# Kernel optimization log

Hardware: AMD Instinct MI355X
Metric: run time of the kernel (lower is better)

The kernel has to match this reference:

```python
import jax, jax.numpy as jnp
import numpy as np

N = 100000   # num_nodes
E = 1600000  # num_edges
H = 128      # hidden_dim
OUT = 1      # output_dim
SLOPE = 0.2  # GATConv leaky_relu negative_slope


def setup_inputs() -> dict:
    key = jax.random.key(0)
    ks = jax.random.split(key, 10)
    s = 1.0 / np.sqrt(H)
    return {
        "h": jnp.arange(N, dtype=jnp.int64 if jax.config.jax_enable_x64 else jnp.int32),
        "edge_index": jax.random.randint(ks[0], (2, E), 0, N),
        "node_type": jax.random.randint(ks[1], (N,), 0, 3),
        "emb": jax.random.normal(ks[2], (N, H), jnp.float32) * s,
        "W1": jax.random.normal(ks[3], (H, H), jnp.float32) * s,
        "a_src1": jax.random.normal(ks[4], (H,), jnp.float32) * s,
        "a_dst1": jax.random.normal(ks[5], (H,), jnp.float32) * s,
        "b1": jnp.zeros((H,), jnp.float32),
        "W2": jax.random.normal(ks[6], (H, OUT), jnp.float32) * s,
        "a_src2": jax.random.normal(ks[7], (OUT,), jnp.float32) * s,
        "a_dst2": jax.random.normal(ks[8], (OUT,), jnp.float32) * s,
        "b2": jnp.zeros((OUT,), jnp.float32),
    }


def gat_layer(x, src, dst, emask, W, a_src, a_dst, b, n_nodes):
    """PyG GATConv (heads=1, add_self_loops=True). Masked edges get -inf logits."""
    xp = x @ W                                  # [N, F]
    e_src = xp @ a_src                          # [N]
    e_dst = xp @ a_dst                          # [N]
    logits = jax.nn.leaky_relu(e_src[src] + e_dst[dst], SLOPE)   # [E]
    logits = jnp.where(emask, logits, -jnp.inf)
    self_logits = jax.nn.leaky_relu(e_src + e_dst, SLOPE)        # [N] self-loops
    # segment softmax over destination nodes (edges + self loop)
    m = jax.ops.segment_max(logits, dst, num_segments=n_nodes)
    m = jnp.maximum(m, self_logits)             # finite: self loop always present
    ew = jnp.exp(logits - m[dst])               # masked edges -> exp(-inf)=0
    sw = jnp.exp(self_logits - m)
    denom = jax.ops.segment_sum(ew, dst, num_segments=n_nodes) + sw
    alpha = ew / denom[dst]                     # [E]
    alpha_self = sw / denom                     # [N]
    out = jax.ops.segment_sum(alpha[:, None] * xp[src], dst, num_segments=n_nodes)
    out = out + alpha_self[:, None] * xp + b
    return out


def reference(h, edge_index, node_type, emb, W1, a_src1, a_dst1, b1, W2, a_src2, a_dst2, b2):
    src, dst = edge_index[0], edge_index[1]
    emask = (node_type[src] == 0) & (node_type[dst] == 0)
    x = emb[h]                                          # embedding lookup [N, H]
    x = gat_layer(x, src, dst, emask, W1, a_src1, a_dst1, b1, emb.shape[0])
    x = jax.nn.relu(x)
    x = gat_layer(x, src, dst, emask, W2, a_src2, a_dst2, b2, emb.shape[0])
    return x
```

## Files before the change

kernel.cpp:

```cpp
#include <hip/hip_runtime.h>

#define N_NODES 100000
#define N_EDGES 1600000
#define HD 128
#define SLOPE 0.2f
#define NBLK 391
#define GB 782
#define EB3 1563
#define CAP 32
#define SLICE_LD 136

typedef __attribute__((ext_vector_type(8))) short bf16x8;
typedef __attribute__((ext_vector_type(4))) float f32x4;

__device__ __forceinline__ unsigned short f2bf(float f) {
    union { float f; unsigned u; } v; v.f = f;
    const unsigned u = v.u + 0x7FFFu + ((v.u >> 16) & 1u);
    return (unsigned short)(u >> 16);
}
__device__ __forceinline__ unsigned pack2(float lo, float hi) {
    return (unsigned)f2bf(lo) | ((unsigned)f2bf(hi) << 16);
}
__device__ __forceinline__ float bf2f(unsigned u16) {
    union { unsigned u; float f; } v; v.u = u16 << 16; return v.f;
}

__global__ __launch_bounds__(256) void k0_zero(
    const int* __restrict__ nt, const float* __restrict__ W1,
    int* __restrict__ deg, unsigned* __restrict__ umask,
    unsigned short* __restrict__ W1bfT)
{
    const int i = blockIdx.x * 256 + threadIdx.x;
    bool act = false;
    if (i < N_NODES) { deg[i] = 0; act = (nt[i] == 0); }
    const unsigned long long bal = __ballot(act);
    const int lane = threadIdx.x & 63;
    if (lane == 0)       umask[i >> 5] = (unsigned)bal;
    else if (lane == 32) umask[i >> 5] = (unsigned)(bal >> 32);
    if (i < HD * HD) {
        const int n = i >> 7, k = i & 127;
        W1bfT[n * HD + k] = f2bf(W1[k * HD + n]);
    }
}

__global__ __launch_bounds__(512) void k1a_edge(
    const int* __restrict__ ei, const unsigned* __restrict__ umask,
    int* __restrict__ deg, int* __restrict__ adj)
{
    const int t = blockIdx.x * 512 + threadIdx.x;
    const int e0 = t * 2;
    if (e0 >= N_EDGES) return;
    const int2 s2 = *(const int2*)(ei + e0);
    const int2 d2 = *(const int2*)(ei + N_EDGES + e0);
    const bool a0 =
        (((umask[s2.x >> 5] >> (s2.x & 31)) & (umask[d2.x >> 5] >> (d2.x & 31))) & 1u) != 0u;
    const bool a1 =
        (((umask[s2.y >> 5] >> (s2.y & 31)) & (umask[d2.y >> 5] >> (d2.y & 31))) & 1u) != 0u;
    if (a0) {
        const int sl = atomicAdd(deg + d2.x, 1);
        if (sl < CAP) adj[(size_t)d2.x * CAP + sl] = s2.x;
    }
    if (a1) {
        const int sl = atomicAdd(deg + d2.y, 1);
        if (sl < CAP) adj[(size_t)d2.y * CAP + sl] = s2.y;
    }
}

__global__ __launch_bounds__(512, 8) void k1b_gemm(
    const int* __restrict__ h,
    const float* __restrict__ emb,
    const unsigned short* __restrict__ W1bfT,
    const float* __restrict__ a_src1,
    const float* __restrict__ a_dst1,
    unsigned short* __restrict__ xp1,
    float* __restrict__ es1,
    float* __restrict__ ed1,
    float* __restrict__ denom1)
{
    __shared__ unsigned short Wlds[8 * 16 * SLICE_LD];
    const int tid = threadIdx.x;

    {
        const int n  = tid >> 2;
        const int kq = (tid & 3) * 32;
        const unsigned short* src = W1bfT + n * HD + kq;
        #pragma unroll
        for (int j = 0; j < 4; ++j) {
            const int c = (kq >> 3) + j;
            const int p = c ^ (n & 7);
            *(bf16x8*)(Wlds + n * HD + p * 8) = *(const bf16x8*)(src + j * 8);
        }
    }

    const int w   = tid >> 6;
    const int L   = tid & 63;
    const int lm  = L & 15;
    const int lg  = L >> 4;
    const int wrow0 = blockIdx.x * 128 + w * 16;

    const int arow = wrow0 + lm;
    const int g = (arow < N_NODES) ? arow : (N_NODES - 1);
    const float* xrow = emb + (size_t)h[g] * HD;

    __syncthreads();

    f32x4 acc[8];
    #pragma unroll
    for (int ct = 0; ct < 8; ++ct) acc[ct] = (f32x4)0.f;

    #pragma unroll
    for (int ks = 0; ks < 4; ++ks) {
        const int k0 = ks * 32 + lg * 8;
        const float4 u = *(const float4*)(xrow + k0);
        const float4 v = *(const float4*)(xrow + k0 + 4);
        union { bf16x8 b; unsigned x[4]; } t;
        t.x[0] = pack2(u.x, u.y);
        t.x[1] = pack2(u.z, u.w);
        t.x[2] = pack2(v.x, v.y);
        t.x[3] = pack2(v.z, v.w);
        const bf16x8 af = t.b;

        const int c = k0 >> 3;
        const int p = (c ^ (lm & 7)) * 8;
        #pragma unroll
        for (int ct = 0; ct < 8; ++ct) {
            const bf16x8 bfr = *(const bf16x8*)(Wlds + (ct * 16 + lm) * HD + p);
            acc[ct] = __builtin_amdgcn_mfma_f32_16x16x32_bf16(af, bfr, acc[ct], 0, 0, 0);
        }
    }

    float asv[8], adv[8];
    #pragma unroll
    for (int ct = 0; ct < 8; ++ct) {
        asv[ct] = a_src1[ct * 16 + lm];
        adv[ct] = a_dst1[ct * 16 + lm];
    }

    #pragma unroll
    for (int reg = 0; reg < 4; ++reg) {
        const int row = wrow0 + lg * 4 + reg;
        float s = 0.f, d = 0.f;
        #pragma unroll
        for (int ct = 0; ct < 8; ++ct) {
            s += acc[ct][reg] * asv[ct];
            d += acc[ct][reg] * adv[ct];
        }
        #pragma unroll
        for (int m = 1; m < 16; m <<= 1) {
            s += __shfl_xor(s, m, 64);
            d += __shfl_xor(d, m, 64);
        }
        if (row < N_NODES && lm == 0) {
            const float sum = s + d;
            const float l = sum > 0.f ? sum : SLOPE * sum;
            es1[row] = s;
            ed1[row] = d;
            denom1[row] = __expf(l);
        }
    }

    __syncthreads();
    unsigned short* slice = Wlds + w * 16 * SLICE_LD;
    #pragma unroll
    for (int ct = 0; ct < 8; ++ct)
        #pragma unroll
        for (int reg = 0; reg < 4; ++reg)
            slice[(lg * 4 + reg) * SLICE_LD + ct * 16 + lm] = f2bf(acc[ct][reg]);
    __syncthreads();
    #pragma unroll
    for (int rr = 0; rr < 4; ++rr) {
        const int rl = rr * 4 + lg;
        const int row = wrow0 + rl;
        if (row < N_NODES) {
            const bf16x8 vdat = *(const bf16x8*)(slice + rl * SLICE_LD + lm * 8);
            *(bf16x8*)(xp1 + (size_t)row * HD + lm * 8) = vdat;
        }
    }
}

__global__ __launch_bounds__(256) void k2_gather(
    const unsigned short* __restrict__ xp1, const float* __restrict__ denom1,
    const float* __restrict__ es1, const float* __restrict__ ed1,
    const int* __restrict__ deg, const int* __restrict__ adj,
    const float* __restrict__ b1, const float* __restrict__ W2,
    float* __restrict__ xp2)
{
    const int wid = threadIdx.x >> 6;
    const int lane = threadIdx.x & 63;
    const int i = blockIdx.x * 4 + wid;
    if (i >= N_NODES) return;

    const int dcount = min(deg[i], CAP);

    const unsigned pself = ((const unsigned*)(xp1 + (size_t)i * HD))[lane];
    float a0 = bf2f(pself & 0xFFFFu);
    float a1 = bf2f(pself >> 16);

    if (dcount > 0) {
        const float wself = denom1[i];
        const float edv   = ed1[i];
        const int* arow = adj + (size_t)i * CAP;

        int nidx = 0; float nw = 0.f;
        if (lane < dcount) {
            nidx = arow[lane];
            const float lgt = es1[nidx] + edv;
            nw = __expf(lgt > 0.f ? lgt : SLOPE * lgt);
        }
        float dsum = nw;
        #pragma unroll
        for (int m = 32; m > 0; m >>= 1) dsum += __shfl_xor(dsum, m, 64);
        const float inv = 1.f / (wself + dsum);

        a0 *= wself;
        a1 *= wself;

        int j = 0;
        for (; j + 2 <= dcount; j += 2) {
            const int   s0 = __shfl(nidx, j, 64);
            const int   s1 = __shfl(nidx, j + 1, 64);
            const float w0 = __shfl(nw, j, 64);
            const float w1 = __shfl(nw, j + 1, 64);
            const unsigned p0 = ((const unsigned*)(xp1 + (size_t)s0 * HD))[lane];
            const unsigned p1 = ((const unsigned*)(xp1 + (size_t)s1 * HD))[lane];
            a0 += w0 * bf2f(p0 & 0xFFFFu) + w1 * bf2f(p1 & 0xFFFFu);
            a1 += w0 * bf2f(p0 >> 16)     + w1 * bf2f(p1 >> 16);
        }
        if (j < dcount) {
            const int   s0 = __shfl(nidx, j, 64);
            const float w0 = __shfl(nw, j, 64);
            const unsigned p0 = ((const unsigned*)(xp1 + (size_t)s0 * HD))[lane];
            a0 += w0 * bf2f(p0 & 0xFFFFu);
            a1 += w0 * bf2f(p0 >> 16);
        }
        a0 *= inv;
        a1 *= inv;
    }

    const float o0 = fmaxf(a0 + b1[2 * lane],     0.f);
    const float o1 = fmaxf(a1 + b1[2 * lane + 1], 0.f);

    float part = o0 * W2[2 * lane] + o1 * W2[2 * lane + 1];
    #pragma unroll
    for (int off = 32; off > 0; off >>= 1) part += __shfl_down(part, off, 64);
    if (lane == 0) xp2[i] = part;
}

__global__ __launch_bounds__(256) void k3_final(
    const float* __restrict__ xp2, const int* __restrict__ deg,
    const int* __restrict__ adj,
    const float* __restrict__ a_src2, const float* __restrict__ a_dst2,
    const float* __restrict__ b2, float* __restrict__ out)
{
    const int i = blockIdx.x * 256 + threadIdx.x;
    if (i >= N_NODES) return;

    const float xi = xp2[i];
    const int dcount = min(deg[i], CAP);
    if (dcount == 0) {
        out[i] = xi + b2[0];
        return;
    }

    const float as = a_src2[0], ad = a_dst2[0];
    const float adxi = ad * xi;
    const float s0 = (as + ad) * xi;
    const float l0 = s0 > 0.f ? s0 : SLOPE * s0;
    const float wself = __expf(l0);

    float denom = wself, num = wself * xi;
    const int* arow = adj + (size_t)i * CAP;

    int j = 0;
    for (; j + 2 <= dcount; j += 2) {
        const int2 ss = *(const int2*)(arow + j);
        const float x0 = xp2[ss.x];
        const float x1 = xp2[ss.y];
        float l0e = as * x0 + adxi; l0e = l0e > 0.f ? l0e : SLOPE * l0e;
        float l1e = as * x1 + adxi; l1e = l1e > 0.f ? l1e : SLOPE * l1e;
        const float w0 = __expf(l0e);
        const float w1 = __expf(l1e);
        denom += w0 + w1;
        num   += w0 * x0 + w1 * x1;
    }
    if (j < dcount) {
        const float x0 = xp2[arow[j]];
        float l0e = as * x0 + adxi; l0e = l0e > 0.f ? l0e : SLOPE * l0e;
        const float w0 = __expf(l0e);
        denom += w0;
        num   += w0 * x0;
    }
    out[i] = num / denom + b2[0];
}

extern "C" void kernel_launch(void* const* d_in, const int* in_sizes, int n_in,
                              void* d_out, int out_size, void* d_ws, size_t ws_size,
                              hipStream_t stream)
{
    const int* h   = (const int*)d_in[0];
    const int* ei  = (const int*)d_in[1];
    const int* nt  = (const int*)d_in[2];
    const float* emb    = (const float*)d_in[3];
    const float* W1     = (const float*)d_in[4];
    const float* a_src1 = (const float*)d_in[5];
    const float* a_dst1 = (const float*)d_in[6];
    const float* b1     = (const float*)d_in[7];
    const float* W2     = (const float*)d_in[8];
    const float* a_src2 = (const float*)d_in[9];
    const float* a_dst2 = (const float*)d_in[10];
    const float* b2     = (const float*)d_in[11];
    float* out = (float*)d_out;

    char* ws = (char*)d_ws;
    size_t off = 0;
    unsigned short* xp1 = (unsigned short*)(ws + off); off += (size_t)N_NODES * HD * sizeof(unsigned short);
    float* es1    = (float*)(ws + off); off += (size_t)N_NODES * sizeof(float);
    float* ed1    = (float*)(ws + off); off += (size_t)N_NODES * sizeof(float);
    float* denom1 = (float*)(ws + off); off += (size_t)N_NODES * sizeof(float);
    float* xp2    = (float*)(ws + off); off += (size_t)N_NODES * sizeof(float);
    int*   deg    = (int*)(ws + off);   off += (size_t)N_NODES * sizeof(int);
    unsigned* umask = (unsigned*)(ws + off); off += 3200 * sizeof(unsigned);
    unsigned short* W1bfT = (unsigned short*)(ws + off); off += (size_t)HD * HD * sizeof(unsigned short);
    off = (off + 255) & ~(size_t)255;
    int*   adj    = (int*)(ws + off);   off += (size_t)N_NODES * CAP * sizeof(int);

    k0_zero<<<NBLK, 256, 0, stream>>>(nt, W1, deg, umask, W1bfT);
    k1a_edge<<<EB3, 512, 0, stream>>>(ei, umask, deg, adj);
    k1b_gemm<<<GB, 512, 0, stream>>>(
        h, emb, W1bfT, a_src1, a_dst1, xp1, es1, ed1, denom1);
    k2_gather<<<(N_NODES + 3) / 4, 256, 0, stream>>>(
        xp1, denom1, es1, ed1, deg, adj, b1, W2, xp2);
    k3_final<<<NBLK, 256, 0, stream>>>(
        xp2, deg, adj, a_src2, a_dst2, b2, out);
}
```

Baseline: 178.2 us.

## Fuse all stages into one persistent kernel with software grid barriers

Replaces the five separate kernel launches with a single persistent kernel of 512 blocks that loops over work and synchronizes stages with an atomic-counter grid barrier. This removes per-launch overhead and the idle gaps between dependent kernels. It also drops the LDS staging of the GEMM output and writes xp1 with scattered 16-bit stores, which may reduce store efficiency. It relies on all blocks being co-resident and adds spin-wait cost at each barrier.

```diff
diff --git a/kernel.cpp b/kernel.cpp
--- a/kernel.cpp
+++ b/kernel.cpp
@@ -4,11 +4,10 @@
 #define N_EDGES 1600000
 #define HD 128
 #define SLOPE 0.2f
-#define NBLK 391
 #define GB 782
-#define EB3 1563
 #define CAP 32
-#define SLICE_LD 136
+#define NN64 100352
+#define NBK 512
 
 typedef __attribute__((ext_vector_type(8))) short bf16x8;
 typedef __attribute__((ext_vector_type(4))) float f32x4;
@@ -25,109 +24,92 @@
     union { unsigned u; float f; } v; v.u = u16 << 16; return v.f;
 }
 
-__global__ __launch_bounds__(256) void k0_zero(
-    const int* __restrict__ nt, const float* __restrict__ W1,
-    int* __restrict__ deg, unsigned* __restrict__ umask,
-    unsigned short* __restrict__ W1bfT)
-{
-    const int i = blockIdx.x * 256 + threadIdx.x;
-    bool act = false;
-    if (i < N_NODES) { deg[i] = 0; act = (nt[i] == 0); }
-    const unsigned long long bal = __ballot(act);
-    const int lane = threadIdx.x & 63;
-    if (lane == 0)       umask[i >> 5] = (unsigned)bal;
-    else if (lane == 32) umask[i >> 5] = (unsigned)(bal >> 32);
-    if (i < HD * HD) {
-        const int n = i >> 7, k = i & 127;
-        W1bfT[n * HD + k] = f2bf(W1[k * HD + n]);
-    }
-}
-
-__global__ __launch_bounds__(512) void k1a_edge(
-    const int* __restrict__ ei, const unsigned* __restrict__ umask,
-    int* __restrict__ deg, int* __restrict__ adj)
-{
-    const int t = blockIdx.x * 512 + threadIdx.x;
-    const int e0 = t * 2;
-    if (e0 >= N_EDGES) return;
-    const int2 s2 = *(const int2*)(ei + e0);
-    const int2 d2 = *(const int2*)(ei + N_EDGES + e0);
-    const bool a0 =
-        (((umask[s2.x >> 5] >> (s2.x & 31)) & (umask[d2.x >> 5] >> (d2.x & 31))) & 1u) != 0u;
-    const bool a1 =
-        (((umask[s2.y >> 5] >> (s2.y & 31)) & (umask[d2.y >> 5] >> (d2.y & 31))) & 1u) != 0u;
-    if (a0) {
-        const int sl = atomicAdd(deg + d2.x, 1);
-        if (sl < CAP) adj[(size_t)d2.x * CAP + sl] = s2.x;
-    }
-    if (a1) {
-        const int sl = atomicAdd(deg + d2.y, 1);
-        if (sl < CAP) adj[(size_t)d2.y * CAP + sl] = s2.y;
-    }
-}
-
-__global__ __launch_bounds__(512, 8) void k1b_gemm(
+__device__ __forceinline__ void gbar(int* bar, int target) {
+    __syncthreads();
+    if (threadIdx.x == 0) {
+        __hip_atomic_fetch_add(bar, 1, __ATOMIC_ACQ_REL, __HIP_MEMORY_SCOPE_AGENT);
+        while (__hip_atomic_load(bar, __ATOMIC_ACQUIRE, __HIP_MEMORY_SCOPE_AGENT) < target) {}
+    }
+    __syncthreads();
+}
+
+__global__ __launch_bounds__(512, 4) void k_mega(
     const int* __restrict__ h,
+    const int* __restrict__ ei,
+    const int* __restrict__ nt,
     const float* __restrict__ emb,
-    const unsigned short* __restrict__ W1bfT,
+    const float* __restrict__ W1,
     const float* __restrict__ a_src1,
     const float* __restrict__ a_dst1,
+    const float* __restrict__ b1,
+    const float* __restrict__ W2,
+    const float* __restrict__ a_src2,
+    const float* __restrict__ a_dst2,
+    const float* __restrict__ b2,
+    float* __restrict__ out,
     unsigned short* __restrict__ xp1,
     float* __restrict__ es1,
     float* __restrict__ ed1,
-    float* __restrict__ denom1)
+    float* __restrict__ denom1,
+    float* __restrict__ xp2,
+    int* __restrict__ deg,
+    unsigned* __restrict__ umask,
+    unsigned short* __restrict__ W1bfT,
+    int* __restrict__ adj,
+    int* __restrict__ bar)
 {
-    __shared__ unsigned short Wlds[8 * 16 * SLICE_LD];
-    const int tid = threadIdx.x;
+    __shared__ unsigned short Wlds[HD * HD];
+    const int tid  = threadIdx.x;
+    const int gt   = (int)blockIdx.x * 512 + tid;
+    const int gstr = NBK * 512;
+    const int w    = tid >> 6;
+    const int lane = tid & 63;
+    const int lm   = lane & 15;
+    const int lg   = lane >> 4;
+
+    if (gt < NN64) {
+        bool act = false;
+        if (gt < N_NODES) { deg[gt] = 0; act = (nt[gt] == 0); }
+        const unsigned long long bal = __ballot(act);
+        if (lane == 0)       umask[gt >> 5] = (unsigned)bal;
+        else if (lane == 32) umask[gt >> 5] = (unsigned)(bal >> 32);
+    }
+    if (gt < HD * HD) {
+        const int n = gt >> 7, k = gt & 127;
+        W1bfT[n * HD + k] = f2bf(W1[k * HD + n]);
+    }
+    gbar(bar, NBK * 1);
+
+    for (int t2 = gt; t2 < (N_EDGES >> 1); t2 += gstr) {
+        const int e0 = t2 << 1;
+        const int2 s2 = *(const int2*)(ei + e0);
+        const int2 d2 = *(const int2*)(ei + N_EDGES + e0);
+        const bool a0 =
+            (((umask[s2.x >> 5] >> (s2.x & 31)) & (umask[d2.x >> 5] >> (d2.x & 31))) & 1u) != 0u;
+        const bool a1 =
+            (((umask[s2.y >> 5] >> (s2.y & 31)) & (umask[d2.y >> 5] >> (d2.y & 31))) & 1u) != 0u;
+        if (a0) {
+            const int sl = atomicAdd(deg + d2.x, 1);
+            if (sl < CAP) adj[(size_t)d2.x * CAP + sl] = s2.x;
+        }
+        if (a1) {
+            const int sl = atomicAdd(deg + d2.y, 1);
+            if (sl < CAP) adj[(size_t)d2.y * CAP + sl] = s2.y;
+        }
+    }
 
     {
         const int n  = tid >> 2;
         const int kq = (tid & 3) * 32;
-        const unsigned short* src = W1bfT + n * HD + kq;
+        const unsigned short* srcp = W1bfT + n * HD + kq;
         #pragma unroll
         for (int j = 0; j < 4; ++j) {
             const int c = (kq >> 3) + j;
             const int p = c ^ (n & 7);
-            *(bf16x8*)(Wlds + n * HD + p * 8) = *(const bf16x8*)(src + j * 8);
-        }
-    }
-
-    const int w   = tid >> 6;
-    const int L   = tid & 63;
-    const int lm  = L & 15;
-    const int lg  = L >> 4;
-    const int wrow0 = blockIdx.x * 128 + w * 16;
-
-    const int arow = wrow0 + lm;
-    const int g = (arow < N_NODES) ? arow : (N_NODES - 1);
-    const float* xrow = emb + (size_t)h[g] * HD;
-
+            *(bf16x8*)(Wlds + n * HD + p * 8) = *(const bf16x8*)(srcp + j * 8);
+        }
+    }
     __syncthreads();
-
-    f32x4 acc[8];
-    #pragma unroll
-    for (int ct = 0; ct < 8; ++ct) acc[ct] = (f32x4)0.f;
-
-    #pragma unroll
-    for (int ks = 0; ks < 4; ++ks) {
-        const int k0 = ks * 32 + lg * 8;
-        const float4 u = *(const float4*)(xrow + k0);
-        const float4 v = *(const float4*)(xrow + k0 + 4);
-        union { bf16x8 b; unsigned x[4]; } t;
-        t.x[0] = pack2(u.x, u.y);
-        t.x[1] = pack2(u.z, u.w);
-        t.x[2] = pack2(v.x, v.y);
-        t.x[3] = pack2(v.z, v.w);
-        const bf16x8 af = t.b;
-
-        const int c = k0 >> 3;
-        const int p = (c ^ (lm & 7)) * 8;
-        #pragma unroll
-        for (int ct = 0; ct < 8; ++ct) {
-            const bf16x8 bfr = *(const bf16x8*)(Wlds + (ct * 16 + lm) * HD + p);
-            acc[ct] = __builtin_amdgcn_mfma_f32_16x16x32_bf16(af, bfr, acc[ct], 0, 0, 0);
-        }
-    }
 
     float asv[8], adv[8];
     #pragma unroll
@@ -136,161 +118,165 @@
         adv[ct] = a_dst1[ct * 16 + lm];
     }
 
-    #pragma unroll
-    for (int reg = 0; reg < 4; ++reg) {
-        const int row = wrow0 + lg * 4 + reg;
-        float s = 0.f, d = 0.f;
-        #pragma unroll
-        for (int ct = 0; ct < 8; ++ct) {
-            s += acc[ct][reg] * asv[ct];
-            d += acc[ct][reg] * adv[ct];
-        }
-        #pragma unroll
-        for (int m = 1; m < 16; m <<= 1) {
-            s += __shfl_xor(s, m, 64);
-            d += __shfl_xor(d, m, 64);
-        }
-        if (row < N_NODES && lm == 0) {
-            const float sum = s + d;
-            const float l = sum > 0.f ? sum : SLOPE * sum;
-            es1[row] = s;
-            ed1[row] = d;
-            denom1[row] = __expf(l);
-        }
-    }
-
-    __syncthreads();
-    unsigned short* slice = Wlds + w * 16 * SLICE_LD;
-    #pragma unroll
-    for (int ct = 0; ct < 8; ++ct)
-        #pragma unroll
-        for (int reg = 0; reg < 4; ++reg)
-            slice[(lg * 4 + reg) * SLICE_LD + ct * 16 + lm] = f2bf(acc[ct][reg]);
-    __syncthreads();
-    #pragma unroll
-    for (int rr = 0; rr < 4; ++rr) {
-        const int rl = rr * 4 + lg;
-        const int row = wrow0 + rl;
-        if (row < N_NODES) {
-            const bf16x8 vdat = *(const bf16x8*)(slice + rl * SLICE_LD + lm * 8);
-            *(bf16x8*)(xp1 + (size_t)row * HD + lm * 8) = vdat;
-        }
-    }
-}
-
-__global__ __launch_bounds__(256) void k2_gather(
-    const unsigned short* __restrict__ xp1, const float* __restrict__ denom1,
-    const float* __restrict__ es1, const float* __restrict__ ed1,
-    const int* __restrict__ deg, const int* __restrict__ adj,
-    const float* __restrict__ b1, const float* __restrict__ W2,
-    float* __restrict__ xp2)
-{
-    const int wid = threadIdx.x >> 6;
-    const int lane = threadIdx.x & 63;
-    const int i = blockIdx.x * 4 + wid;
-    if (i >= N_NODES) return;
-
-    const int dcount = min(deg[i], CAP);
-
-    const unsigned pself = ((const unsigned*)(xp1 + (size_t)i * HD))[lane];
-    float a0 = bf2f(pself & 0xFFFFu);
-    float a1 = bf2f(pself >> 16);
-
-    if (dcount > 0) {
-        const float wself = denom1[i];
-        const float edv   = ed1[i];
+    for (int vb = blockIdx.x; vb < GB; vb += NBK) {
+        const int wrow0 = vb * 128 + w * 16;
+        const int arow = wrow0 + lm;
+        const int g = (arow < N_NODES) ? arow : (N_NODES - 1);
+        const float* xrow = emb + (size_t)h[g] * HD;
+
+        f32x4 acc[8];
+        #pragma unroll
+        for (int ct = 0; ct < 8; ++ct) acc[ct] = (f32x4)0.f;
+
+        #pragma unroll
+        for (int ks = 0; ks < 4; ++ks) {
+            const int k0 = ks * 32 + lg * 8;
+            const float4 u = *(const float4*)(xrow + k0);
+            const float4 v = *(const float4*)(xrow + k0 + 4);
+            union { bf16x8 b; unsigned x[4]; } t;
+            t.x[0] = pack2(u.x, u.y);
+            t.x[1] = pack2(u.z, u.w);
+            t.x[2] = pack2(v.x, v.y);
+            t.x[3] = pack2(v.z, v.w);
+            const bf16x8 af = t.b;
+
+            const int c = k0 >> 3;
+            const int p = (c ^ (lm & 7)) * 8;
+            #pragma unroll
+            for (int ct = 0; ct < 8; ++ct) {
+                const bf16x8 bfr = *(const bf16x8*)(Wlds + (ct * 16 + lm) * HD + p);
+                acc[ct] = __builtin_amdgcn_mfma_f32_16x16x32_bf16(af, bfr, acc[ct], 0, 0, 0);
+            }
+        }
+
+        #pragma unroll
+        for (int reg = 0; reg < 4; ++reg) {
+            const int row = wrow0 + lg * 4 + reg;
+            float s = 0.f, d = 0.f;
+            #pragma unroll
+            for (int ct = 0; ct < 8; ++ct) {
+                s += acc[ct][reg] * asv[ct];
+                d += acc[ct][reg] * adv[ct];
+            }
+            #pragma unroll
+            for (int m = 1; m < 16; m <<= 1) {
+                s += __shfl_xor(s, m, 64);
+                d += __shfl_xor(d, m, 64);
+            }
+            if (row < N_NODES) {
+                unsigned short* dstp = xp1 + (size_t)row * HD;
+                #pragma unroll
+                for (int ct = 0; ct < 8; ++ct)
+                    dstp[ct * 16 + lm] = f2bf(acc[ct][reg]);
+                if (lm == 0) {
+                    const float sum = s + d;
+                    const float l = sum > 0.f ? sum : SLOPE * sum;
+                    es1[row] = s;
+                    ed1[row] = d;
+                    denom1[row] = __expf(l);
+                }
+            }
+        }
+    }
+    gbar(bar, NBK * 2);
+
+    for (int i = (int)blockIdx.x * 8 + w; i < N_NODES; i += NBK * 8) {
+        const int dcount = min(deg[i], CAP);
+
+        const unsigned pself = ((const unsigned*)(xp1 + (size_t)i * HD))[lane];
+        float a0 = bf2f(pself & 0xFFFFu);
+        float a1 = bf2f(pself >> 16);
+
+        if (dcount > 0) {
+            const float wself = denom1[i];
+            const float edv   = ed1[i];
+            const int* arow = adj + (size_t)i * CAP;
+
+            int nidx = 0; float nw = 0.f;
+            if (lane < dcount) {
+                nidx = arow[lane];
+                const float lgt = es1[nidx] + edv;
+                nw = __expf(lgt > 0.f ? lgt : SLOPE * lgt);
+            }
+            float dsum = nw;
+            #pragma unroll
+            for (int m = 32; m > 0; m >>= 1) dsum += __shfl_xor(dsum, m, 64);
+            const float inv = 1.f / (wself + dsum);
+
+            a0 *= wself;
+            a1 *= wself;
+
+            int j = 0;
+            for (; j + 2 <= dcount; j += 2) {
+                const int   s0 = __shfl(nidx, j, 64);
+                const int   s1 = __shfl(nidx, j + 1, 64);
+                const float w0 = __shfl(nw, j, 64);
+                const float w1 = __shfl(nw, j + 1, 64);
+                const unsigned p0 = ((const unsigned*)(xp1 + (size_t)s0 * HD))[lane];
+                const unsigned p1 = ((const unsigned*)(xp1 + (size_t)s1 * HD))[lane];
+                a0 += w0 * bf2f(p0 & 0xFFFFu) + w1 * bf2f(p1 & 0xFFFFu);
+                a1 += w0 * bf2f(p0 >> 16)     + w1 * bf2f(p1 >> 16);
+            }
+            if (j < dcount) {
+                const int   s0 = __shfl(nidx, j, 64);
+                const float w0 = __shfl(nw, j, 64);
+                const unsigned p0 = ((const unsigned*)(xp1 + (size_t)s0 * HD))[lane];
+                a0 += w0 * bf2f(p0 & 0xFFFFu);
+                a1 += w0 * bf2f(p0 >> 16);
+            }
+            a0 *= inv;
+            a1 *= inv;
+        }
+
+        const float o0 = fmaxf(a0 + b1[2 * lane],     0.f);
+        const float o1 = fmaxf(a1 + b1[2 * lane + 1], 0.f);
+
+        float part = o0 * W2[2 * lane] + o1 * W2[2 * lane + 1];
+        #pragma unroll
+        for (int off = 32; off > 0; off >>= 1) part += __shfl_down(part, off, 64);
+        if (lane == 0) xp2[i] = part;
+    }
+    gbar(bar, NBK * 3);
+
+    if (gt < N_NODES) {
+        const int i = gt;
+        const float xi = xp2[i];
+        const int dcount = min(deg[i], CAP);
+        if (dcount == 0) {
+            out[i] = xi + b2[0];
+            return;
+        }
+
+        const float as = a_src2[0], ad = a_dst2[0];
+        const float adxi = ad * xi;
+        const float s0 = (as + ad) * xi;
+        const float l0 = s0 > 0.f ? s0 : SLOPE * s0;
+        const float wself = __expf(l0);
+
+        float denom = wself, num = wself * xi;
         const int* arow = adj + (size_t)i * CAP;
-
-        int nidx = 0; float nw = 0.f;
-        if (lane < dcount) {
-            nidx = arow[lane];
-            const float lgt = es1[nidx] + edv;
-            nw = __expf(lgt > 0.f ? lgt : SLOPE * lgt);
-        }
-        float dsum = nw;
-        #pragma unroll
-        for (int m = 32; m > 0; m >>= 1) dsum += __shfl_xor(dsum, m, 64);
-        const float inv = 1.f / (wself + dsum);
-
-        a0 *= wself;
-        a1 *= wself;
 
         int j = 0;
         for (; j + 2 <= dcount; j += 2) {
-            const int   s0 = __shfl(nidx, j, 64);
-            const int   s1 = __shfl(nidx, j + 1, 64);
-            const float w0 = __shfl(nw, j, 64);
-            const float w1 = __shfl(nw, j + 1, 64);
-            const unsigned p0 = ((const unsigned*)(xp1 + (size_t)s0 * HD))[lane];
-            const unsigned p1 = ((const unsigned*)(xp1 + (size_t)s1 * HD))[lane];
-            a0 += w0 * bf2f(p0 & 0xFFFFu) + w1 * bf2f(p1 & 0xFFFFu);
-            a1 += w0 * bf2f(p0 >> 16)     + w1 * bf2f(p1 >> 16);
+            const int2 ss = *(const int2*)(arow + j);
+            const float x0 = xp2[ss.x];
+            const float x1 = xp2[ss.y];
+            float l0e = as * x0 + adxi; l0e = l0e > 0.f ? l0e : SLOPE * l0e;
+            float l1e = as * x1 + adxi; l1e = l1e > 0.f ? l1e : SLOPE * l1e;
+            const float w0 = __expf(l0e);
+            const float w1 = __expf(l1e);
+            denom += w0 + w1;
+            num   += w0 * x0 + w1 * x1;
         }
         if (j < dcount) {
-            const int   s0 = __shfl(nidx, j, 64);
-            const float w0 = __shfl(nw, j, 64);
-            const unsigned p0 = ((const unsigned*)(xp1 + (size_t)s0 * HD))[lane];
-            a0 += w0 * bf2f(p0 & 0xFFFFu);
-            a1 += w0 * bf2f(p0 >> 16);
-        }
-        a0 *= inv;
-        a1 *= inv;
-    }
-
-    const float o0 = fmaxf(a0 + b1[2 * lane],     0.f);
-    const float o1 = fmaxf(a1 + b1[2 * lane + 1], 0.f);
-
-    float part = o0 * W2[2 * lane] + o1 * W2[2 * lane + 1];
-    #pragma unroll
-    for (int off = 32; off > 0; off >>= 1) part += __shfl_down(part, off, 64);
-    if (lane == 0) xp2[i] = part;
-}
-
-__global__ __launch_bounds__(256) void k3_final(
-    const float* __restrict__ xp2, const int* __restrict__ deg,
-    const int* __restrict__ adj,
-    const float* __restrict__ a_src2, const float* __restrict__ a_dst2,
-    const float* __restrict__ b2, float* __restrict__ out)
-{
-    const int i = blockIdx.x * 256 + threadIdx.x;
-    if (i >= N_NODES) return;
-
-    const float xi = xp2[i];
-    const int dcount = min(deg[i], CAP);
-    if (dcount == 0) {
-        out[i] = xi + b2[0];
-        return;
-    }
-
-    const float as = a_src2[0], ad = a_dst2[0];
-    const float adxi = ad * xi;
-    const float s0 = (as + ad) * xi;
-    const float l0 = s0 > 0.f ? s0 : SLOPE * s0;
-    const float wself = __expf(l0);
-
-    float denom = wself, num = wself * xi;
-    const int* arow = adj + (size_t)i * CAP;
-
-    int j = 0;
-    for (; j + 2 <= dcount; j += 2) {
-        const int2 ss = *(const int2*)(arow + j);
-        const float x0 = xp2[ss.x];
-        const float x1 = xp2[ss.y];
-        float l0e = as * x0 + adxi; l0e = l0e > 0.f ? l0e : SLOPE * l0e;
-        float l1e = as * x1 + adxi; l1e = l1e > 0.f ? l1e : SLOPE * l1e;
-        const float w0 = __expf(l0e);
-        const float w1 = __expf(l1e);
-        denom += w0 + w1;
-        num   += w0 * x0 + w1 * x1;
-    }
-    if (j < dcount) {
-        const float x0 = xp2[arow[j]];
-        float l0e = as * x0 + adxi; l0e = l0e > 0.f ? l0e : SLOPE * l0e;
-        const float w0 = __expf(l0e);
-        denom += w0;
-        num   += w0 * x0;
-    }
-    out[i] = num / denom + b2[0];
+            const float x0 = xp2[arow[j]];
+            float l0e = as * x0 + adxi; l0e = l0e > 0.f ? l0e : SLOPE * l0e;
+            const float w0 = __expf(l0e);
+            denom += w0;
+            num   += w0 * x0;
+        }
+        out[i] = num / denom + b2[0];
+    }
 }
 
 extern "C" void kernel_launch(void* const* d_in, const int* in_sizes, int n_in,
@@ -323,13 +309,11 @@
     unsigned short* W1bfT = (unsigned short*)(ws + off); off += (size_t)HD * HD * sizeof(unsigned short);
     off = (off + 255) & ~(size_t)255;
     int*   adj    = (int*)(ws + off);   off += (size_t)N_NODES * CAP * sizeof(int);
-
-    k0_zero<<<NBLK, 256, 0, stream>>>(nt, W1, deg, umask, W1bfT);
-    k1a_edge<<<EB3, 512, 0, stream>>>(ei, umask, deg, adj);
-    k1b_gemm<<<GB, 512, 0, stream>>>(
-        h, emb, W1bfT, a_src1, a_dst1, xp1, es1, ed1, denom1);
-    k2_gather<<<(N_NODES + 3) / 4, 256, 0, stream>>>(
-        xp1, denom1, es1, ed1, deg, adj, b1, W2, xp2);
-    k3_final<<<NBLK, 256, 0, stream>>>(
-        xp2, deg, adj, a_src2, a_dst2, b2, out);
-}
+    off = (off + 255) & ~(size_t)255;
+    int*   bar    = (int*)(ws + off);   off += 256;
+
+    hipMemsetAsync(bar, 0, sizeof(int), stream);
+    k_mega<<<NBK, 512, 0, stream>>>(
+        h, ei, nt, emb, W1, a_src1, a_dst1, b1, W2, a_src2, a_dst2, b2, out,
+        xp1, es1, ed1, denom1, xp2, deg, umask, W1bfT, adj, bar);
+}
```

After: 471.9 us. 165% more time.

## Skip xp1 writes and gather for nodes without active in-edges

Applied to the files above, without the earlier changes.

Removes the k0 prep kernel: deg and a new source-mask are zeroed with a memset, edge masks read node_type directly, and the W1 bf16 transpose is done inside the GEMM block. The GEMM epilogue now computes the layer-2 projection for isolated nodes directly and writes xp1 only for nodes that are destinations or active sources, so k2 can return early for zero-degree nodes. This cuts xp1 write traffic and gather work for the large fraction of nodes that are masked, but adds atomicOr traffic in the edge kernel, redundant per-block W1 conversion with strided loads, and uncoalesced scalar bf16 stores instead of staged vector stores.

```diff
diff --git a/kernel.cpp b/kernel.cpp
--- a/kernel.cpp
+++ b/kernel.cpp
@@ -8,7 +8,6 @@
 #define GB 782
 #define EB3 1563
 #define CAP 32
-#define SLICE_LD 136
 
 typedef __attribute__((ext_vector_type(8))) short bf16x8;
 typedef __attribute__((ext_vector_type(4))) float f32x4;
@@ -25,70 +24,61 @@
     union { unsigned u; float f; } v; v.u = u16 << 16; return v.f;
 }
 
-__global__ __launch_bounds__(256) void k0_zero(
-    const int* __restrict__ nt, const float* __restrict__ W1,
-    int* __restrict__ deg, unsigned* __restrict__ umask,
-    unsigned short* __restrict__ W1bfT)
-{
-    const int i = blockIdx.x * 256 + threadIdx.x;
-    bool act = false;
-    if (i < N_NODES) { deg[i] = 0; act = (nt[i] == 0); }
-    const unsigned long long bal = __ballot(act);
-    const int lane = threadIdx.x & 63;
-    if (lane == 0)       umask[i >> 5] = (unsigned)bal;
-    else if (lane == 32) umask[i >> 5] = (unsigned)(bal >> 32);
-    if (i < HD * HD) {
-        const int n = i >> 7, k = i & 127;
-        W1bfT[n * HD + k] = f2bf(W1[k * HD + n]);
-    }
-}
-
 __global__ __launch_bounds__(512) void k1a_edge(
-    const int* __restrict__ ei, const unsigned* __restrict__ umask,
-    int* __restrict__ deg, int* __restrict__ adj)
+    const int* __restrict__ ei, const int* __restrict__ nt,
+    int* __restrict__ deg, unsigned* __restrict__ srcmask,
+    int* __restrict__ adj)
 {
     const int t = blockIdx.x * 512 + threadIdx.x;
     const int e0 = t * 2;
     if (e0 >= N_EDGES) return;
     const int2 s2 = *(const int2*)(ei + e0);
     const int2 d2 = *(const int2*)(ei + N_EDGES + e0);
-    const bool a0 =
-        (((umask[s2.x >> 5] >> (s2.x & 31)) & (umask[d2.x >> 5] >> (d2.x & 31))) & 1u) != 0u;
-    const bool a1 =
-        (((umask[s2.y >> 5] >> (s2.y & 31)) & (umask[d2.y >> 5] >> (d2.y & 31))) & 1u) != 0u;
+    const bool a0 = (nt[s2.x] == 0) && (nt[d2.x] == 0);
+    const bool a1 = (nt[s2.y] == 0) && (nt[d2.y] == 0);
     if (a0) {
         const int sl = atomicAdd(deg + d2.x, 1);
         if (sl < CAP) adj[(size_t)d2.x * CAP + sl] = s2.x;
+        atomicOr(srcmask + (s2.x >> 5), 1u << (s2.x & 31));
     }
     if (a1) {
         const int sl = atomicAdd(deg + d2.y, 1);
         if (sl < CAP) adj[(size_t)d2.y * CAP + sl] = s2.y;
+        atomicOr(srcmask + (s2.y >> 5), 1u << (s2.y & 31));
     }
 }
 
 __global__ __launch_bounds__(512, 8) void k1b_gemm(
     const int* __restrict__ h,
     const float* __restrict__ emb,
-    const unsigned short* __restrict__ W1bfT,
+    const float* __restrict__ W1,
     const float* __restrict__ a_src1,
     const float* __restrict__ a_dst1,
+    const float* __restrict__ b1,
+    const float* __restrict__ W2,
+    const int* __restrict__ deg,
+    const unsigned* __restrict__ srcmask,
     unsigned short* __restrict__ xp1,
     float* __restrict__ es1,
     float* __restrict__ ed1,
-    float* __restrict__ denom1)
-{
-    __shared__ unsigned short Wlds[8 * 16 * SLICE_LD];
+    float* __restrict__ denom1,
+    float* __restrict__ xp2)
+{
+    __shared__ unsigned short Wlds[HD * HD];
     const int tid = threadIdx.x;
 
     {
         const int n  = tid >> 2;
         const int kq = (tid & 3) * 32;
-        const unsigned short* src = W1bfT + n * HD + kq;
         #pragma unroll
         for (int j = 0; j < 4; ++j) {
+            union { bf16x8 b; unsigned short u[8]; } tmp;
+            #pragma unroll
+            for (int kk = 0; kk < 8; ++kk)
+                tmp.u[kk] = f2bf(W1[(kq + j * 8 + kk) * HD + n]);
             const int c = (kq >> 3) + j;
             const int p = c ^ (n & 7);
-            *(bf16x8*)(Wlds + n * HD + p * 8) = *(const bf16x8*)(src + j * 8);
+            *(bf16x8*)(Wlds + n * HD + p * 8) = tmp.b;
         }
     }
 
@@ -129,51 +119,59 @@
         }
     }
 
-    float asv[8], adv[8];
+    float asv[8], adv[8], b1v[8], w2v[8];
     #pragma unroll
     for (int ct = 0; ct < 8; ++ct) {
         asv[ct] = a_src1[ct * 16 + lm];
         adv[ct] = a_dst1[ct * 16 + lm];
+        b1v[ct] = b1[ct * 16 + lm];
+        w2v[ct] = W2[ct * 16 + lm];
     }
 
     #pragma unroll
     for (int reg = 0; reg < 4; ++reg) {
         const int row = wrow0 + lg * 4 + reg;
-        float s = 0.f, d = 0.f;
+        float s = 0.f, d = 0.f, p = 0.f;
         #pragma unroll
         for (int ct = 0; ct < 8; ++ct) {
-            s += acc[ct][reg] * asv[ct];
-            d += acc[ct][reg] * adv[ct];
+            const float a = acc[ct][reg];
+            s += a * asv[ct];
+            d += a * adv[ct];
+            p += fmaxf(a + b1v[ct], 0.f) * w2v[ct];
         }
         #pragma unroll
         for (int m = 1; m < 16; m <<= 1) {
             s += __shfl_xor(s, m, 64);
             d += __shfl_xor(d, m, 64);
-        }
-        if (row < N_NODES && lm == 0) {
-            const float sum = s + d;
-            const float l = sum > 0.f ? sum : SLOPE * sum;
-            es1[row] = s;
-            ed1[row] = d;
-            denom1[row] = __expf(l);
-        }
-    }
-
-    __syncthreads();
-    unsigned short* slice = Wlds + w * 16 * SLICE_LD;
-    #pragma unroll
-    for (int ct = 0; ct < 8; ++ct)
-        #pragma unroll
-        for (int reg = 0; reg < 4; ++reg)
-            slice[(lg * 4 + reg) * SLICE_LD + ct * 16 + lm] = f2bf(acc[ct][reg]);
-    __syncthreads();
-    #pragma unroll
-    for (int rr = 0; rr < 4; ++rr) {
-        const int rl = rr * 4 + lg;
-        const int row = wrow0 + rl;
+            p += __shfl_xor(p, m, 64);
+        }
         if (row < N_NODES) {
-            const bf16x8 vdat = *(const bf16x8*)(slice + rl * SLICE_LD + lm * 8);
-            *(bf16x8*)(xp1 + (size_t)row * HD + lm * 8) = vdat;
+            const int dcnt = deg[row];
+            if (dcnt == 0) {
+                if (lm == 0) {
+                    xp2[row] = p;
+                    es1[row] = s;
+                }
+                const bool issrc = ((srcmask[row >> 5] >> (row & 31)) & 1u) != 0u;
+                if (issrc) {
+                    unsigned short* dstp = xp1 + (size_t)row * HD;
+                    #pragma unroll
+                    for (int ct = 0; ct < 8; ++ct)
+                        dstp[ct * 16 + lm] = f2bf(acc[ct][reg]);
+                }
+            } else {
+                unsigned short* dstp = xp1 + (size_t)row * HD;
+                #pragma unroll
+                for (int ct = 0; ct < 8; ++ct)
+                    dstp[ct * 16 + lm] = f2bf(acc[ct][reg]);
+                if (lm == 0) {
+                    const float sum = s + d;
+                    const float l = sum > 0.f ? sum : SLOPE * sum;
+                    es1[row] = s;
+                    ed1[row] = d;
+                    denom1[row] = __expf(l);
+                }
+            }
         }
     }
 }
@@ -191,51 +189,47 @@
     if (i >= N_NODES) return;
 
     const int dcount = min(deg[i], CAP);
+    if (dcount == 0) return;
+
+    const float wself = denom1[i];
+    const float edv   = ed1[i];
+    const int* arow = adj + (size_t)i * CAP;
+
+    int nidx = 0; float nw = 0.f;
+    if (lane < dcount) {
+        nidx = arow[lane];
+        const float lgt = es1[nidx] + edv;
+        nw = __expf(lgt > 0.f ? lgt : SLOPE * lgt);
+    }
+    float dsum = nw;
+    #pragma unroll
+    for (int m = 32; m > 0; m >>= 1) dsum += __shfl_xor(dsum, m, 64);
+    const float inv = 1.f / (wself + dsum);
 
     const unsigned pself = ((const unsigned*)(xp1 + (size_t)i * HD))[lane];
-    float a0 = bf2f(pself & 0xFFFFu);
-    float a1 = bf2f(pself >> 16);
-
-    if (dcount > 0) {
-        const float wself = denom1[i];
-        const float edv   = ed1[i];
-        const int* arow = adj + (size_t)i * CAP;
-
-        int nidx = 0; float nw = 0.f;
-        if (lane < dcount) {
-            nidx = arow[lane];
-            const float lgt = es1[nidx] + edv;
-            nw = __expf(lgt > 0.f ? lgt : SLOPE * lgt);
-        }
-        float dsum = nw;
-        #pragma unroll
-        for (int m = 32; m > 0; m >>= 1) dsum += __shfl_xor(dsum, m, 64);
-        const float inv = 1.f / (wself + dsum);
-
-        a0 *= wself;
-        a1 *= wself;
-
-        int j = 0;
-        for (; j + 2 <= dcount; j += 2) {
-            const int   s0 = __shfl(nidx, j, 64);
-            const int   s1 = __shfl(nidx, j + 1, 64);
-            const float w0 = __shfl(nw, j, 64);
-            const float w1 = __shfl(nw, j + 1, 64);
-            const unsigned p0 = ((const unsigned*)(xp1 + (size_t)s0 * HD))[lane];
-            const unsigned p1 = ((const unsigned*)(xp1 + (size_t)s1 * HD))[lane];
-            a0 += w0 * bf2f(p0 & 0xFFFFu) + w1 * bf2f(p1 & 0xFFFFu);
-            a1 += w0 * bf2f(p0 >> 16)     + w1 * bf2f(p1 >> 16);
-        }
-        if (j < dcount) {
-            const int   s0 = __shfl(nidx, j, 64);
-            const float w0 = __shfl(nw, j, 64);
-            const unsigned p0 = ((const unsigned*)(xp1 + (size_t)s0 * HD))[lane];
-            a0 += w0 * bf2f(p0 & 0xFFFFu);
-            a1 += w0 * bf2f(p0 >> 16);
-        }
-        a0 *= inv;
-        a1 *= inv;
-    }
+    float a0 = wself * bf2f(pself & 0xFFFFu);
+    float a1 = wself * bf2f(pself >> 16);
+
+    int j = 0;
+    for (; j + 2 <= dcount; j += 2) {
+        const int   s0 = __shfl(nidx, j, 64);
+        const int   s1 = __shfl(nidx, j + 1, 64);
+        const float w0 = __shfl(nw, j, 64);
+        const float w1 = __shfl(nw, j + 1, 64);
+        const unsigned p0 = ((const unsigned*)(xp1 + (size_t)s0 * HD))[lane];
+        const unsigned p1 = ((const unsigned*)(xp1 + (size_t)s1 * HD))[lane];
+        a0 += w0 * bf2f(p0 & 0xFFFFu) + w1 * bf2f(p1 & 0xFFFFu);
+        a1 += w0 * bf2f(p0 >> 16)     + w1 * bf2f(p1 >> 16);
+    }
+    if (j < dcount) {
+        const int   s0 = __shfl(nidx, j, 64);
+        const float w0 = __shfl(nw, j, 64);
+        const unsigned p0 = ((const unsigned*)(xp1 + (size_t)s0 * HD))[lane];
+        a0 += w0 * bf2f(p0 & 0xFFFFu);
+        a1 += w0 * bf2f(p0 >> 16);
+    }
+    a0 *= inv;
+    a1 *= inv;
 
     const float o0 = fmaxf(a0 + b1[2 * lane],     0.f);
     const float o1 = fmaxf(a1 + b1[2 * lane + 1], 0.f);
@@ -319,15 +313,16 @@
     float* denom1 = (float*)(ws + off); off += (size_t)N_NODES * sizeof(float);
     float* xp2    = (float*)(ws + off); off += (size_t)N_NODES * sizeof(float);
     int*   deg    = (int*)(ws + off);   off += (size_t)N_NODES * sizeof(int);
-    unsigned* umask = (unsigned*)(ws + off); off += 3200 * sizeof(unsigned);
-    unsigned short* W1bfT = (unsigned short*)(ws + off); off += (size_t)HD * HD * sizeof(unsigned short);
+    unsigned* srcmask = (unsigned*)(ws + off); off += 3200 * sizeof(unsigned);
     off = (off + 255) & ~(size_t)255;
     int*   adj    = (int*)(ws + off);   off += (size_t)N_NODES * CAP * sizeof(int);
 
-    k0_zero<<<NBLK, 256, 0, stream>>>(nt, W1, deg, umask, W1bfT);
-    k1a_edge<<<EB3, 512, 0, stream>>>(ei, umask, deg, adj);
+    hipMemsetAsync(deg, 0, (size_t)(N_NODES + 3200) * sizeof(int), stream);
+
+    k1a_edge<<<EB3, 512, 0, stream>>>(ei, nt, deg, srcmask, adj);
     k1b_gemm<<<GB, 512, 0, stream>>>(
-        h, emb, W1bfT, a_src1, a_dst1, xp1, es1, ed1, denom1);
+        h, emb, W1, a_src1, a_dst1, b1, W2, deg, srcmask,
+        xp1, es1, ed1, denom1, xp2);
     k2_gather<<<(N_NODES + 3) / 4, 256, 0, stream>>>(
         xp1, denom1, es1, ed1, deg, adj, b1, W2, xp2);
     k3_final<<<NBLK, 256, 0, stream>>>(
```

New measurement: 262.6 us. +47.3%, slower.

## Skip gather and xp1 writes for isolated nodes via GEMM-fused layer-2 projection

Applied to the files above, without the earlier changes.

Nodes with no active incoming edges now get their layer-2 projection (relu(xp1+b1)·W2) computed directly in the GEMM epilogue, and the gather kernel returns early for them. A source bitmask built with atomicOr during edge bucketing lets the GEMM skip writing xp1 rows that are neither destinations nor sources of active edges. This cuts gather work and xp1 write traffic, since roughly two thirds of nodes are not type 0, in exchange for extra atomics in the edge kernel and deg/mask reads in the GEMM.

```diff
diff --git a/kernel.cpp b/kernel.cpp
--- a/kernel.cpp
+++ b/kernel.cpp
@@ -28,7 +28,7 @@
 __global__ __launch_bounds__(256) void k0_zero(
     const int* __restrict__ nt, const float* __restrict__ W1,
     int* __restrict__ deg, unsigned* __restrict__ umask,
-    unsigned short* __restrict__ W1bfT)
+    unsigned* __restrict__ srcmask, unsigned short* __restrict__ W1bfT)
 {
     const int i = blockIdx.x * 256 + threadIdx.x;
     bool act = false;
@@ -37,6 +37,7 @@
     const int lane = threadIdx.x & 63;
     if (lane == 0)       umask[i >> 5] = (unsigned)bal;
     else if (lane == 32) umask[i >> 5] = (unsigned)(bal >> 32);
+    if (i < 3200) srcmask[i] = 0u;
     if (i < HD * HD) {
         const int n = i >> 7, k = i & 127;
         W1bfT[n * HD + k] = f2bf(W1[k * HD + n]);
@@ -45,7 +46,8 @@
 
 __global__ __launch_bounds__(512) void k1a_edge(
     const int* __restrict__ ei, const unsigned* __restrict__ umask,
-    int* __restrict__ deg, int* __restrict__ adj)
+    int* __restrict__ deg, unsigned* __restrict__ srcmask,
+    int* __restrict__ adj)
 {
     const int t = blockIdx.x * 512 + threadIdx.x;
     const int e0 = t * 2;
@@ -59,10 +61,12 @@
     if (a0) {
         const int sl = atomicAdd(deg + d2.x, 1);
         if (sl < CAP) adj[(size_t)d2.x * CAP + sl] = s2.x;
+        atomicOr(srcmask + (s2.x >> 5), 1u << (s2.x & 31));
     }
     if (a1) {
         const int sl = atomicAdd(deg + d2.y, 1);
         if (sl < CAP) adj[(size_t)d2.y * CAP + sl] = s2.y;
+        atomicOr(srcmask + (s2.y >> 5), 1u << (s2.y & 31));
     }
 }
 
@@ -72,10 +76,15 @@
     const unsigned short* __restrict__ W1bfT,
     const float* __restrict__ a_src1,
     const float* __restrict__ a_dst1,
+    const float* __restrict__ b1,
+    const float* __restrict__ W2,
+    const int* __restrict__ deg,
+    const unsigned* __restrict__ srcmask,
     unsigned short* __restrict__ xp1,
     float* __restrict__ es1,
     float* __restrict__ ed1,
-    float* __restrict__ denom1)
+    float* __restrict__ denom1,
+    float* __restrict__ xp2)
 {
     __shared__ unsigned short Wlds[8 * 16 * SLICE_LD];
     const int tid = threadIdx.x;
@@ -83,12 +92,12 @@
     {
         const int n  = tid >> 2;
         const int kq = (tid & 3) * 32;
-        const unsigned short* src = W1bfT + n * HD + kq;
+        const unsigned short* srcp = W1bfT + n * HD + kq;
         #pragma unroll
         for (int j = 0; j < 4; ++j) {
             const int c = (kq >> 3) + j;
             const int p = c ^ (n & 7);
-            *(bf16x8*)(Wlds + n * HD + p * 8) = *(const bf16x8*)(src + j * 8);
+            *(bf16x8*)(Wlds + n * HD + p * 8) = *(const bf16x8*)(srcp + j * 8);
         }
     }
 
@@ -129,33 +138,42 @@
         }
     }
 
-    float asv[8], adv[8];
+    float asv[8], adv[8], b1v[8], w2v[8];
     #pragma unroll
     for (int ct = 0; ct < 8; ++ct) {
         asv[ct] = a_src1[ct * 16 + lm];
         adv[ct] = a_dst1[ct * 16 + lm];
+        b1v[ct] = b1[ct * 16 + lm];
+        w2v[ct] = W2[ct * 16 + lm];
     }
 
     #pragma unroll
     for (int reg = 0; reg < 4; ++reg) {
         const int row = wrow0 + lg * 4 + reg;
-        float s = 0.f, d = 0.f;
+        float s = 0.f, d = 0.f, p = 0.f;
         #pragma unroll
         for (int ct = 0; ct < 8; ++ct) {
-            s += acc[ct][reg] * asv[ct];
-            d += acc[ct][reg] * adv[ct];
+            const float a = acc[ct][reg];
+            s += a * asv[ct];
+            d += a * adv[ct];
+            p += fmaxf(a + b1v[ct], 0.f) * w2v[ct];
         }
         #pragma unroll
         for (int m = 1; m < 16; m <<= 1) {
             s += __shfl_xor(s, m, 64);
             d += __shfl_xor(d, m, 64);
+            p += __shfl_xor(p, m, 64);
         }
         if (row < N_NODES && lm == 0) {
-            const float sum = s + d;
-            const float l = sum > 0.f ? sum : SLOPE * sum;
             es1[row] = s;
-            ed1[row] = d;
-            denom1[row] = __expf(l);
+            if (deg[row] == 0) {
+                xp2[row] = p;
+            } else {
+                const float sum = s + d;
+                const float l = sum > 0.f ? sum : SLOPE * sum;
+                ed1[row] = d;
+                denom1[row] = __expf(l);
+            }
         }
     }
 
@@ -172,8 +190,12 @@
         const int rl = rr * 4 + lg;
         const int row = wrow0 + rl;
         if (row < N_NODES) {
-            const bf16x8 vdat = *(const bf16x8*)(slice + rl * SLICE_LD + lm * 8);
-            *(bf16x8*)(xp1 + (size_t)row * HD + lm * 8) = vdat;
+            const bool need = (deg[row] > 0) ||
+                (((srcmask[row >> 5] >> (row & 31)) & 1u) != 0u);
+            if (need) {
+                const bf16x8 vdat = *(const bf16x8*)(slice + rl * SLICE_LD + lm * 8);
+                *(bf16x8*)(xp1 + (size_t)row * HD + lm * 8) = vdat;
+            }
         }
     }
 }
@@ -191,51 +213,47 @@
     if (i >= N_NODES) return;
 
     const int dcount = min(deg[i], CAP);
+    if (dcount == 0) return;
+
+    const float wself = denom1[i];
+    const float edv   = ed1[i];
+    const int* arow = adj + (size_t)i * CAP;
+
+    int nidx = 0; float nw = 0.f;
+    if (lane < dcount) {
+        nidx = arow[lane];
+        const float lgt = es1[nidx] + edv;
+        nw = __expf(lgt > 0.f ? lgt : SLOPE * lgt);
+    }
+    float dsum = nw;
+    #pragma unroll
+    for (int m = 32; m > 0; m >>= 1) dsum += __shfl_xor(dsum, m, 64);
+    const float inv = 1.f / (wself + dsum);
 
     const unsigned pself = ((const unsigned*)(xp1 + (size_t)i * HD))[lane];
-    float a0 = bf2f(pself & 0xFFFFu);
-    float a1 = bf2f(pself >> 16);
-
-    if (dcount > 0) {
-        const float wself = denom1[i];
-        const float edv   = ed1[i];
-        const int* arow = adj + (size_t)i * CAP;
-
-        int nidx = 0; float nw = 0.f;
-        if (lane < dcount) {
-            nidx = arow[lane];
-            const float lgt = es1[nidx] + edv;
-            nw = __expf(lgt > 0.f ? lgt : SLOPE * lgt);
-        }
-        float dsum = nw;
-        #pragma unroll
-        for (int m = 32; m > 0; m >>= 1) dsum += __shfl_xor(dsum, m, 64);
-        const float inv = 1.f / (wself + dsum);
-
-        a0 *= wself;
-        a1 *= wself;
-
-        int j = 0;
-        for (; j + 2 <= dcount; j += 2) {
-            const int   s0 = __shfl(nidx, j, 64);
-            const int   s1 = __shfl(nidx, j + 1, 64);
-            const float w0 = __shfl(nw, j, 64);
-            const float w1 = __shfl(nw, j + 1, 64);
-            const unsigned p0 = ((const unsigned*)(xp1 + (size_t)s0 * HD))[lane];
-            const unsigned p1 = ((const unsigned*)(xp1 + (size_t)s1 * HD))[lane];
-            a0 += w0 * bf2f(p0 & 0xFFFFu) + w1 * bf2f(p1 & 0xFFFFu);
-            a1 += w0 * bf2f(p0 >> 16)     + w1 * bf2f(p1 >> 16);
-        }
-        if (j < dcount) {
-            const int   s0 = __shfl(nidx, j, 64);
-            const float w0 = __shfl(nw, j, 64);
-            const unsigned p0 = ((const unsigned*)(xp1 + (size_t)s0 * HD))[lane];
-            a0 += w0 * bf2f(p0 & 0xFFFFu);
-            a1 += w0 * bf2f(p0 >> 16);
-        }
-        a0 *= inv;
-        a1 *= inv;
-    }
+    float a0 = wself * bf2f(pself & 0xFFFFu);
+    float a1 = wself * bf2f(pself >> 16);
+
+    int j = 0;
+    for (; j + 2 <= dcount; j += 2) {
+        const int   s0 = __shfl(nidx, j, 64);
+        const int   s1 = __shfl(nidx, j + 1, 64);
+        const float w0 = __shfl(nw, j, 64);
+        const float w1 = __shfl(nw, j + 1, 64);
+        const unsigned p0 = ((const unsigned*)(xp1 + (size_t)s0 * HD))[lane];
+        const unsigned p1 = ((const unsigned*)(xp1 + (size_t)s1 * HD))[lane];
+        a0 += w0 * bf2f(p0 & 0xFFFFu) + w1 * bf2f(p1 & 0xFFFFu);
+        a1 += w0 * bf2f(p0 >> 16)     + w1 * bf2f(p1 >> 16);
+    }
+    if (j < dcount) {
+        const int   s0 = __shfl(nidx, j, 64);
+        const float w0 = __shfl(nw, j, 64);
+        const unsigned p0 = ((const unsigned*)(xp1 + (size_t)s0 * HD))[lane];
+        a0 += w0 * bf2f(p0 & 0xFFFFu);
+        a1 += w0 * bf2f(p0 >> 16);
+    }
+    a0 *= inv;
+    a1 *= inv;
 
     const float o0 = fmaxf(a0 + b1[2 * lane],     0.f);
     const float o1 = fmaxf(a1 + b1[2 * lane + 1], 0.f);
@@ -319,15 +337,17 @@
     float* denom1 = (float*)(ws + off); off += (size_t)N_NODES * sizeof(float);
     float* xp2    = (float*)(ws + off); off += (size_t)N_NODES * sizeof(float);
     int*   deg    = (int*)(ws + off);   off += (size_t)N_NODES * sizeof(int);
-    unsigned* umask = (unsigned*)(ws + off); off += 3200 * sizeof(unsigned);
+    unsigned* umask   = (unsigned*)(ws + off); off += 3200 * sizeof(unsigned);
+    unsigned* srcmask = (unsigned*)(ws + off); off += 3200 * sizeof(unsigned);
     unsigned short* W1bfT = (unsigned short*)(ws + off); off += (size_t)HD * HD * sizeof(unsigned short);
     off = (off + 255) & ~(size_t)255;
     int*   adj    = (int*)(ws + off);   off += (size_t)N_NODES * CAP * sizeof(int);
 
-    k0_zero<<<NBLK, 256, 0, stream>>>(nt, W1, deg, umask, W1bfT);
-    k1a_edge<<<EB3, 512, 0, stream>>>(ei, umask, deg, adj);
+    k0_zero<<<NBLK, 256, 0, stream>>>(nt, W1, deg, umask, srcmask, W1bfT);
+    k1a_edge<<<EB3, 512, 0, stream>>>(ei, umask, deg, srcmask, adj);
     k1b_gemm<<<GB, 512, 0, stream>>>(
-        h, emb, W1bfT, a_src1, a_dst1, xp1, es1, ed1, denom1);
+        h, emb, W1bfT, a_src1, a_dst1, b1, W2, deg, srcmask,
+        xp1, es1, ed1, denom1, xp2);
     k2_gather<<<(N_NODES + 3) / 4, 256, 0, stream>>>(
         xp1, denom1, es1, ed1, deg, adj, b1, W2, xp2);
     k3_final<<<NBLK, 256, 0, stream>>>(
```

Result: slower. 222.4 us (+24.8%).
